# Kernel tuning notes

Hardware: AMD Instinct MI355X
Metric: run time of the kernel (lower is better)

## Reference

```python
import jax
import jax.numpy as jnp
import numpy as np

B, S, D, H, HID, E, TOPK = 1, 2048, 1024, 16, 4096, 8, 2
HEAD_DIM = D // H


def _layer_norm(x, g, b, eps=1e-5):
    mu = jnp.mean(x, axis=-1, keepdims=True)
    var = jnp.var(x, axis=-1, keepdims=True)
    return (x - mu) * jax.lax.rsqrt(var + eps) * g + b


def setup_inputs() -> dict:
    key = jax.random.key(0)
    ks = jax.random.split(key, 12)
    s = 0.02
    return {
        "x": jax.random.normal(ks[0], (B, S, D), jnp.float32),
        "ln1_g": jnp.ones((D,), jnp.float32),
        "ln1_b": jnp.zeros((D,), jnp.float32),
        "wq": jax.random.normal(ks[1], (D, D), jnp.float32) * s,
        "wk": jax.random.normal(ks[2], (D, D), jnp.float32) * s,
        "wv": jax.random.normal(ks[3], (D, D), jnp.float32) * s,
        "wo": jax.random.normal(ks[4], (D, D), jnp.float32) * s,
        "ln2_g": jnp.ones((D,), jnp.float32),
        "ln2_b": jnp.zeros((D,), jnp.float32),
        "w_gate": jax.random.normal(ks[5], (D, E), jnp.float32) * s,
        "w_eg": jax.random.normal(ks[6], (E, D, HID), jnp.float32) * s,
        "w_eu": jax.random.normal(ks[7], (E, D, HID), jnp.float32) * s,
        "w_ed": jax.random.normal(ks[8], (E, HID, D), jnp.float32) * s,
    }


def _attention(h, wq, wk, wv, wo):
    b, s, d = h.shape
    q = (h @ wq).reshape(b, s, H, HEAD_DIM).transpose(0, 2, 1, 3)
    k = (h @ wk).reshape(b, s, H, HEAD_DIM).transpose(0, 2, 1, 3)
    v = (h @ wv).reshape(b, s, H, HEAD_DIM).transpose(0, 2, 1, 3)
    scores = jnp.einsum("bhqd,bhkd->bhqk", q, k) / jnp.sqrt(jnp.asarray(HEAD_DIM, h.dtype))
    causal = jnp.tril(jnp.ones((s, s), bool))  # [s,s]
    scores = jnp.where(causal, scores, jnp.asarray(-1e30, h.dtype))
    attn = jax.nn.softmax(scores, axis=-1)
    out = jnp.einsum("bhqk,bhkd->bhqd", attn, v).transpose(0, 2, 1, 3).reshape(b, s, d)
    return out @ wo


def _moe(h, w_gate, w_eg, w_eu, w_ed):
    b, s, d = h.shape
    flat = h.reshape(-1, d)  # [T,D]
    logits = flat @ w_gate  # [T,E]
    scores = jax.nn.sigmoid(logits)
    top_val, top_idx = jax.lax.top_k(scores, TOPK)
    top_val = top_val / (jnp.sum(top_val, axis=-1, keepdims=True) + 1e-9)
    # per-token per-expert combine weight (0 for unrouted experts)
    combine = jnp.sum(jax.nn.one_hot(top_idx, E, dtype=flat.dtype) * top_val[..., None], axis=1)  # [T,E]
    g = jax.nn.silu(jnp.einsum("td,edh->eth", flat, w_eg))
    u = jnp.einsum("td,edh->eth", flat, w_eu)
    eo = jnp.einsum("eth,ehd->etd", g * u, w_ed)  # [E,T,D]
    out = jnp.einsum("etd,te->td", eo, combine)
    return out.reshape(b, s, d)


def reference(x, ln1_g, ln1_b, wq, wk, wv, wo, ln2_g, ln2_b, w_gate, w_eg, w_eu, w_ed):
    x = x + _attention(_layer_norm(x, ln1_g, ln1_b), wq, wk, wv, wo)
    x = x + _moe(_layer_norm(x, ln2_g, ln2_b), w_gate, w_eg, w_eu, w_ed)
    return x
```

## Files before the change

kernel.cpp:

```cpp
#include <hip/hip_runtime.h>
#include <hip/hip_bf16.h>
#include <stdint.h>

#define DI __device__ __forceinline__

typedef short bf16x8_t __attribute__((ext_vector_type(8)));
typedef float f32x4_t __attribute__((ext_vector_type(4)));

DI unsigned short f2bf(float f) {
  __hip_bfloat16 h = __float2bfloat16(f);
  unsigned short u;
  __builtin_memcpy(&u, &h, 2);
  return u;
}

DI uint32_t pk2(float a, float b) {
  return (uint32_t)f2bf(a) | ((uint32_t)f2bf(b) << 16);
}

DI f32x4_t mfma16(bf16x8_t a, bf16x8_t b, f32x4_t c) {
  return __builtin_amdgcn_mfma_f32_16x16x32_bf16(a, b, c, 0, 0, 0);
}

DI void gload16(const void* g, void* l) {
  __builtin_amdgcn_global_load_lds(
      (const __attribute__((address_space(1))) uint32_t*)g,
      (__attribute__((address_space(3))) uint32_t*)l, 16, 0, 0);
}

DI bf16x8_t frag(const unsigned short* base, int row, int hi) {
  return *(const bf16x8_t*)&base[row * 32 + ((hi ^ ((row >> 1) & 3)) * 8)];
}
DI int chunk_swz(int tid) { return ((tid & 3) ^ ((tid >> 3) & 3)) * 8; }

__global__ __launch_bounds__(256) void transpose_cvt(const float* __restrict__ in,
                                                     unsigned short* __restrict__ out,
                                                     int R, int C) {
  __shared__ float tile[64][65];
  const int tid = threadIdx.x;
  const int tx = tid & 15, ty = tid >> 4;
  const size_t zoff = (size_t)blockIdx.z * R * C;
  const int r0 = blockIdx.y * 64, c0 = blockIdx.x * 64;
#pragma unroll
  for (int i = 0; i < 4; ++i) {
    const int r = ty + i * 16;
    const float4 v = *(const float4*)(in + zoff + (size_t)(r0 + r) * C + c0 + tx * 4);
    tile[r][tx * 4 + 0] = v.x; tile[r][tx * 4 + 1] = v.y;
    tile[r][tx * 4 + 2] = v.z; tile[r][tx * 4 + 3] = v.w;
  }
  __syncthreads();
#pragma unroll
  for (int i = 0; i < 4; ++i) {
    const int r = ty + i * 16;
    ushort4 o;
    o.x = f2bf(tile[tx * 4 + 0][r]); o.y = f2bf(tile[tx * 4 + 1][r]);
    o.z = f2bf(tile[tx * 4 + 2][r]); o.w = f2bf(tile[tx * 4 + 3][r]);
    *(ushort4*)(out + zoff + (size_t)(c0 + r) * R + r0 + tx * 4) = o;
  }
}

__global__ __launch_bounds__(256) void ln_kernel(const float* __restrict__ x, const float* __restrict__ g,
                                                 const float* __restrict__ b, unsigned short* __restrict__ out) {
  const int row = blockIdx.x, tid = threadIdx.x;
  const int wid = tid >> 6, lane = tid & 63;
  const float4 v = *(const float4*)(x + (size_t)row * 1024 + tid * 4);
  float s = v.x + v.y + v.z + v.w;
  float s2 = v.x * v.x + v.y * v.y + v.z * v.z + v.w * v.w;
#pragma unroll
  for (int o = 1; o < 64; o <<= 1) { s += __shfl_xor(s, o); s2 += __shfl_xor(s2, o); }
  __shared__ float red[8];
  if (lane == 0) { red[wid] = s; red[4 + wid] = s2; }
  __syncthreads();
  const float ts = red[0] + red[1] + red[2] + red[3];
  const float ts2 = red[4] + red[5] + red[6] + red[7];
  const float mu = ts * 0.0009765625f;
  const float var = ts2 * 0.0009765625f - mu * mu;
  const float rs = rsqrtf(var + 1e-5f);
  const float4 gg = *(const float4*)(g + tid * 4);
  const float4 bb = *(const float4*)(b + tid * 4);
  ushort4 o4;
  o4.x = f2bf((v.x - mu) * rs * gg.x + bb.x);
  o4.y = f2bf((v.y - mu) * rs * gg.y + bb.y);
  o4.z = f2bf((v.z - mu) * rs * gg.z + bb.z);
  o4.w = f2bf((v.w - mu) * rs * gg.w + bb.w);
  *(ushort4*)(out + (size_t)row * 1024 + tid * 4) = o4;
}

template<int BN>
DI void gemm_loop(const unsigned short* aR0, const unsigned short* aR1,
                  const unsigned short* bR0, const unsigned short* bR1,
                  const int K, unsigned short* lds, const int tid,
                  f32x4_t (&acc)[4][BN / 32]) {
  constexpr int NF = BN / 32;
  unsigned short* ldsA = lds;
  unsigned short* ldsB = lds + 4096;
  const int wid = tid >> 6, lane = tid & 63, ln = lane & 15, hi = lane >> 4;
  const int wr = wid >> 1, wc = wid & 1;
  char* dstA0 = (char*)ldsA + wid * 1024;
  char* dstA1 = (char*)ldsA + 4096 + wid * 1024;
  char* dstB0 = (char*)ldsB + wid * 1024;
  char* dstB1 = (char*)ldsB + 4096 + wid * 1024;
  for (int k0 = 0; k0 < K; k0 += 32) {
    gload16(aR0 + k0, dstA0);
    gload16(aR1 + k0, dstA1);
    gload16(bR0 + k0, dstB0);
    if constexpr (BN == 128) gload16(bR1 + k0, dstB1);
    __syncthreads();
    bf16x8_t af[4];
#pragma unroll
    for (int mf = 0; mf < 4; ++mf)
      af[mf] = frag(ldsA, wr * 64 + mf * 16 + ln, hi);
#pragma unroll
    for (int nf = 0; nf < NF; ++nf) {
      bf16x8_t bfr = frag(ldsB, wc * (BN / 2) + nf * 16 + ln, hi);
#pragma unroll
      for (int mf = 0; mf < 4; ++mf)
        acc[mf][nf] = mfma16(af[mf], bfr, acc[mf][nf]);
    }
    __syncthreads();
  }
}

__global__ __launch_bounds__(256) void qkv_kernel(const unsigned short* __restrict__ h1,
                                                  const unsigned short* __restrict__ wqT,
                                                  const unsigned short* __restrict__ wkT,
                                                  const unsigned short* __restrict__ wvT,
                                                  unsigned short* __restrict__ qb,
                                                  unsigned short* __restrict__ kbf,
                                                  unsigned short* __restrict__ vt) {
  __shared__ unsigned short lds[128 * 32 + 128 * 32];
  const int tid = threadIdx.x;
  const int z = blockIdx.z;
  const unsigned short* BT = (z == 0) ? wqT : (z == 1) ? wkT : wvT;
  const int m0 = blockIdx.y * 128, n0 = blockIdx.x * 128;
  f32x4_t acc[4][4] = {};
  const int cs = chunk_swz(tid);
  const unsigned short* aR0 = h1 + (size_t)(m0 + (tid >> 2)) * 1024 + cs;
  const unsigned short* aR1 = aR0 + 64 * 1024;
  const unsigned short* bR0 = BT + (size_t)(n0 + (tid >> 2)) * 1024 + cs;
  const unsigned short* bR1 = bR0 + 64 * 1024;
  gemm_loop<128>(aR0, aR1, bR0, bR1, 1024, lds, tid, acc);
  const int lane = tid & 63, ln = lane & 15, hi = lane >> 4, wid = tid >> 6;
  const int wr = wid >> 1, wc = wid & 1;
  if (z < 2) {
    unsigned short* o = z ? kbf : qb;
#pragma unroll
    for (int mf = 0; mf < 4; ++mf)
#pragma unroll
      for (int nf = 0; nf < 4; ++nf)
#pragma unroll
        for (int r = 0; r < 4; ++r) {
          const int m = m0 + wr * 64 + mf * 16 + hi * 4 + r;
          const int n = n0 + wc * 64 + nf * 16 + ln;
          o[(size_t)m * 1024 + n] = f2bf(acc[mf][nf][r]);
        }
  } else {
#pragma unroll
    for (int mf = 0; mf < 4; ++mf)
#pragma unroll
      for (int nf = 0; nf < 4; ++nf) {
        const int n = n0 + wc * 64 + nf * 16 + ln;
        const int mb = m0 + wr * 64 + mf * 16 + hi * 4;
        ushort4 o;
        o.x = f2bf(acc[mf][nf][0]); o.y = f2bf(acc[mf][nf][1]);
        o.z = f2bf(acc[mf][nf][2]); o.w = f2bf(acc[mf][nf][3]);
        *(ushort4*)(vt + (size_t)n * 2048 + mb) = o;
      }
  }
}

__global__ __launch_bounds__(256) void wo_kernel(const unsigned short* __restrict__ ao,
                                                 const unsigned short* __restrict__ woT,
                                                 const float* __restrict__ x,
                                                 float* __restrict__ out) {
  __shared__ unsigned short lds[128 * 32 + 64 * 32];
  const int tid = threadIdx.x;
  const int m0 = blockIdx.y * 128, n0 = blockIdx.x * 64;
  f32x4_t acc[4][2] = {};
  const int cs = chunk_swz(tid);
  const unsigned short* aR0 = ao + (size_t)(m0 + (tid >> 2)) * 1024 + cs;
  const unsigned short* aR1 = aR0 + 64 * 1024;
  const unsigned short* bR0 = woT + (size_t)(n0 + (tid >> 2)) * 1024 + cs;
  gemm_loop<64>(aR0, aR1, bR0, nullptr, 1024, lds, tid, acc);
  const int lane = tid & 63, ln = lane & 15, hi = lane >> 4, wid = tid >> 6;
  const int wr = wid >> 1, wc = wid & 1;
#pragma unroll
  for (int mf = 0; mf < 4; ++mf)
#pragma unroll
    for (int nf = 0; nf < 2; ++nf)
#pragma unroll
      for (int r = 0; r < 4; ++r) {
        const int m = m0 + wr * 64 + mf * 16 + hi * 4 + r;
        const int n = n0 + wc * 32 + nf * 16 + ln;
        out[(size_t)m * 1024 + n] = acc[mf][nf][r] + x[(size_t)m * 1024 + n];
      }
}

__global__ __launch_bounds__(256) void attn_kernel(const unsigned short* __restrict__ qb,
                                                   const unsigned short* __restrict__ kbuf,
                                                   const unsigned short* __restrict__ vt,
                                                   unsigned short* __restrict__ ao) {
  __shared__ unsigned short kTl[4096];
  __shared__ unsigned short vTl[4096];
  __shared__ unsigned short pl[4][1024];
  const int tid = threadIdx.x;
  const int wid = tid >> 6, lane = tid & 63;
  const int ln = lane & 15, hi = lane >> 4;
  const int h = blockIdx.y;
  const int q0 = blockIdx.x * 64;
  const int q0w = q0 + wid * 16;

  const unsigned short* qrow = qb + (size_t)(q0w + ln) * 1024 + h * 64 + hi * 8;
  const bf16x8_t aq0 = *(const bf16x8_t*)(qrow);
  const bf16x8_t aq1 = *(const bf16x8_t*)(qrow + 32);

  const int str_r = tid >> 3, str_c = tid & 7;
  const int swc = (str_c ^ (str_r & 7)) * 8;
  const unsigned short* ksrc0 = kbuf + (size_t)str_r * 1024 + h * 64 + swc;
  const unsigned short* ksrc1 = kbuf + (size_t)(str_r + 32) * 1024 + h * 64 + swc;
  const unsigned short* vsrc0 = vt + (size_t)(h * 64 + str_r) * 2048 + swc;
  const unsigned short* vsrc1 = vt + (size_t)(h * 64 + str_r + 32) * 2048 + swc;
  char* kd0 = (char*)kTl + wid * 1024;
  char* kd1 = (char*)kTl + 4096 + wid * 1024;
  char* vd0 = (char*)vTl + wid * 1024;
  char* vd1 = (char*)vTl + 4096 + wid * 1024;

  float m_r[4], l_r[4];
  f32x4_t o_acc[4] = {};
#pragma unroll
  for (int r = 0; r < 4; ++r) { m_r[r] = -1e30f; l_r[r] = 0.f; }

  const int nkv = blockIdx.x + 1;
  for (int it = 0; it < nkv; ++it) {
    const int kv0 = it * 64;
    gload16(ksrc0 + (size_t)kv0 * 1024, kd0);
    gload16(ksrc1 + (size_t)kv0 * 1024, kd1);
    gload16(vsrc0 + kv0, vd0);
    gload16(vsrc1 + kv0, vd1);
    __syncthreads();

    float sc[4][4];
#pragma unroll
    for (int cf = 0; cf < 4; ++cf) {
      const int row = cf * 16 + ln;
      const int swz = row & 7;
      const bf16x8_t b0 = *(const bf16x8_t*)((char*)kTl + row * 128 + ((hi ^ swz) * 16));
      const bf16x8_t b1 = *(const bf16x8_t*)((char*)kTl + row * 128 + (((4 + hi) ^ swz) * 16));
      f32x4_t zacc = {};
      zacc = mfma16(aq0, b0, zacc);
      zacc = mfma16(aq1, b1, zacc);
#pragma unroll
      for (int r = 0; r < 4; ++r) sc[cf][r] = zacc[r] * 0.125f;
    }
    if (kv0 + 63 > q0w) {
#pragma unroll
      for (int cf = 0; cf < 4; ++cf)
#pragma unroll
        for (int r = 0; r < 4; ++r) {
          const int qg = q0w + hi * 4 + r;
          const int kg = kv0 + cf * 16 + ln;
          if (kg > qg) sc[cf][r] = -1e30f;
        }
    }
#pragma unroll
    for (int r = 0; r < 4; ++r) {
      float tm = fmaxf(fmaxf(sc[0][r], sc[1][r]), fmaxf(sc[2][r], sc[3][r]));
      tm = fmaxf(tm, __shfl_xor(tm, 1));
      tm = fmaxf(tm, __shfl_xor(tm, 2));
      tm = fmaxf(tm, __shfl_xor(tm, 4));
      tm = fmaxf(tm, __shfl_xor(tm, 8));
      const float mn = fmaxf(m_r[r], tm);
      const float alpha = __expf(m_r[r] - mn);
      float rsum = 0.f;
#pragma unroll
      for (int cf = 0; cf < 4; ++cf) {
        const float p = __expf(sc[cf][r] - mn);
        sc[cf][r] = p; rsum += p;
      }
      rsum += __shfl_xor(rsum, 1); rsum += __shfl_xor(rsum, 2);
      rsum += __shfl_xor(rsum, 4); rsum += __shfl_xor(rsum, 8);
      l_r[r] = l_r[r] * alpha + rsum;
      m_r[r] = mn;
#pragma unroll
      for (int df = 0; df < 4; ++df) o_acc[df][r] *= alpha;
    }
    unsigned short* pw = &pl[wid][0];
#pragma unroll
    for (int cf = 0; cf < 4; ++cf)
#pragma unroll
      for (int r = 0; r < 4; ++r) {
        const int qq = hi * 4 + r;
        const int kv = cf * 16 + ln;
        const int bo = (qq * 128 + kv * 2) ^ ((qq & 7) << 4);
        *(unsigned short*)((char*)pw + bo) = f2bf(sc[cf][r]);
      }
    __syncthreads();
    const bf16x8_t pa0 = *(const bf16x8_t*)((char*)pw + ((ln * 128 + hi * 16) ^ ((ln & 7) << 4)));
    const bf16x8_t pa1 = *(const bf16x8_t*)((char*)pw + ((ln * 128 + 64 + hi * 16) ^ ((ln & 7) << 4)));
#pragma unroll
    for (int df = 0; df < 4; ++df) {
      const int d = df * 16 + ln;
      const int swz = d & 7;
      const bf16x8_t bv0 = *(const bf16x8_t*)((char*)vTl + d * 128 + ((hi ^ swz) * 16));
      const bf16x8_t bv1 = *(const bf16x8_t*)((char*)vTl + d * 128 + (((4 + hi) ^ swz) * 16));
      o_acc[df] = mfma16(pa0, bv0, o_acc[df]);
      o_acc[df] = mfma16(pa1, bv1, o_acc[df]);
    }
    __syncthreads();
  }
#pragma unroll
  for (int df = 0; df < 4; ++df) {
    const int n = h * 64 + df * 16 + ln;
#pragma unroll
    for (int r = 0; r < 4; ++r) {
      const int m = q0w + hi * 4 + r;
      ao[(size_t)m * 1024 + n] = f2bf(o_acc[df][r] / l_r[r]);
    }
  }
}

__global__ __launch_bounds__(256) void gate_kernel(const float* __restrict__ x2, const float* __restrict__ g,
                                                   const float* __restrict__ b, const float* __restrict__ wg,
                                                   int2* __restrict__ te, float2* __restrict__ tw,
                                                   int* __restrict__ cnt) {
  const int tid = threadIdx.x, wid = tid >> 6, lane = tid & 63;
  const int t = blockIdx.x * 4 + wid;
  const float* row = x2 + (size_t)t * 1024;
  float vv[16];
#pragma unroll
  for (int i = 0; i < 4; ++i) *(float4*)&vv[i * 4] = *(const float4*)(row + lane * 16 + i * 4);
  float s = 0.f, s2 = 0.f;
#pragma unroll
  for (int j = 0; j < 16; ++j) { s += vv[j]; s2 += vv[j] * vv[j]; }
#pragma unroll
  for (int o = 1; o < 64; o <<= 1) { s += __shfl_xor(s, o); s2 += __shfl_xor(s2, o); }
  const float mu = s * 0.0009765625f;
  const float var = s2 * 0.0009765625f - mu * mu;
  const float rs = rsqrtf(var + 1e-5f);
  float acc[8] = {0.f, 0.f, 0.f, 0.f, 0.f, 0.f, 0.f, 0.f};
#pragma unroll
  for (int j = 0; j < 16; ++j) {
    const int d = lane * 16 + j;
    const float xv = (vv[j] - mu) * rs * g[d] + b[d];
    const float4 w0 = *(const float4*)(wg + d * 8);
    const float4 w1 = *(const float4*)(wg + d * 8 + 4);
    acc[0] += xv * w0.x; acc[1] += xv * w0.y; acc[2] += xv * w0.z; acc[3] += xv * w0.w;
    acc[4] += xv * w1.x; acc[5] += xv * w1.y; acc[6] += xv * w1.z; acc[7] += xv * w1.w;
  }
#pragma unroll
  for (int o = 1; o < 64; o <<= 1) {
#pragma unroll
    for (int e = 0; e < 8; ++e) acc[e] += __shfl_xor(acc[e], o);
  }
  if (lane == 0) {
    float sg[8];
#pragma unroll
    for (int e = 0; e < 8; ++e) sg[e] = 1.f / (1.f + __expf(-acc[e]));
    int e0 = 0;
#pragma unroll
    for (int e = 1; e < 8; ++e) if (sg[e] > sg[e0]) e0 = e;
    int e1 = (e0 == 0) ? 1 : 0;
#pragma unroll
    for (int e = 0; e < 8; ++e) if (e != e0 && sg[e] > sg[e1]) e1 = e;
    const float v0 = sg[e0], v1 = sg[e1];
    const float inv = 1.f / (v0 + v1 + 1e-9f);
    te[t] = make_int2(e0, e1);
    tw[t] = make_float2(v0 * inv, v1 * inv);
    atomicAdd(&cnt[e0], 1);
    atomicAdd(&cnt[e1], 1);
  }
}

__global__ void zero_counters(int* p) { if (threadIdx.x < 8) p[threadIdx.x] = 0; }

__global__ void g2_kernel(const int* __restrict__ cnt, int* __restrict__ slot_off,
                          int* __restrict__ tile_expert, int* __restrict__ tile_rowbase,
                          int* __restrict__ cursor, int* __restrict__ assign_token,
                          float* __restrict__ assign_w) {
  const int tid = threadIdx.x;
  for (int i = tid; i < 5120; i += 64) { assign_token[i] = -1; assign_w[i] = 0.f; }
  if (tid == 0) {
    int base = 0, tiles = 0;
    for (int e = 0; e < 8; ++e) {
      const int c = cnt[e];
      slot_off[e] = base;
      cursor[e] = 0;
      const int nt = (c + 127) >> 7;
      for (int i = 0; i < nt; ++i) {
        tile_expert[tiles] = e;
        tile_rowbase[tiles] = base + i * 128;
        ++tiles;
      }
      base += nt * 128;
    }
    for (; tiles < 40; ++tiles) tile_expert[tiles] = -1;
  }
}

__global__ __launch_bounds__(256) void g3_kernel(const int2* __restrict__ te, const float2* __restrict__ tw,
                                                 const int* __restrict__ slot_off, int* __restrict__ cursor,
                                                 int* __restrict__ assign_token, float* __restrict__ assign_w) {
  const int t = blockIdx.x * 256 + threadIdx.x;
  const int2 e = te[t];
  const float2 w = tw[t];
  const int s0 = slot_off[e.x] + atomicAdd(&cursor[e.x], 1);
  assign_token[s0] = t; assign_w[s0] = w.x;
  const int s1 = slot_off[e.y] + atomicAdd(&cursor[e.y], 1);
  assign_token[s1] = t; assign_w[s1] = w.y;
}

__global__ __launch_bounds__(256) void upgate_kernel(const unsigned short* __restrict__ h2,
                                                     const float* __restrict__ w_eg, const float* __restrict__ w_eu,
                                                     const int* __restrict__ tile_expert,
                                                     const int* __restrict__ tile_rowbase,
                                                     const int* __restrict__ assign_token,
                                                     unsigned short* __restrict__ act) {
  const int by = blockIdx.y;
  const int e = tile_expert[by];
  if (e < 0) return;
  const int n0 = blockIdx.x * 64;
  const int rowbase = tile_rowbase[by];
  const int tid = threadIdx.x;
  __shared__ unsigned short lds[2 * 4096 + 2 * 4096];
  unsigned short* ldsA = lds;
  unsigned short* ldsB = lds + 8192;
  const int wid = tid >> 6, lane = tid & 63, ln = lane & 15, hi = lane >> 4;
  const int wr = wid >> 1, wc = wid & 1;
  const int r0s = rowbase + (tid >> 2);
  int t0 = assign_token[r0s];       t0 = t0 < 0 ? 0 : t0;
  int t1 = assign_token[r0s + 64];  t1 = t1 < 0 ? 0 : t1;
  const int cs = chunk_swz(tid);
  const unsigned short* aR0 = h2 + (size_t)t0 * 1024 + cs;
  const unsigned short* aR1 = h2 + (size_t)t1 * 1024 + cs;
  const int mat = tid >> 7;
  const int blk = tid & 127;
  const int kb = (blk >> 4) * 4;
  const int nb = (blk & 15) * 4;
  const float* bsrc = (mat ? w_eu : w_eg) + (size_t)e * 1024 * 4096 + (size_t)kb * 4096 + n0 + nb;
  int boff[4];
#pragma unroll
  for (int i = 0; i < 4; ++i) {
    const int n = nb + i;
    int bo = mat * 4096 + n * 64 + kb * 2;
    bo ^= ((n >> 2) & 7) << 4;
    boff[i] = bo;
  }
  f32x4_t accg[4][2] = {};
  f32x4_t accu[4][2] = {};
  gload16(aR0, (char*)ldsA + wid * 1024);
  gload16(aR1, (char*)ldsA + 4096 + wid * 1024);
  {
    const float4 q0 = *(const float4*)(bsrc);
    const float4 q1 = *(const float4*)(bsrc + 4096);
    const float4 q2 = *(const float4*)(bsrc + 8192);
    const float4 q3 = *(const float4*)(bsrc + 12288);
    const float* q0p = (const float*)&q0; const float* q1p = (const float*)&q1;
    const float* q2p = (const float*)&q2; const float* q3p = (const float*)&q3;
#pragma unroll
    for (int i = 0; i < 4; ++i) {
      uint2 w;
      w.x = pk2(q0p[i], q1p[i]);
      w.y = pk2(q2p[i], q3p[i]);
      *(uint2*)((char*)ldsB + boff[i]) = w;
    }
  }
  __syncthreads();
  int buf = 0;
  for (int k0 = 0; k0 < 1024; k0 += 32) {
    const int kn = k0 + 32;
    const int nbuf = buf ^ 1;
    const bool pf = kn < 1024;
    float4 q0, q1, q2, q3;
    if (pf) {
      gload16(aR0 + kn, (char*)ldsA + nbuf * 8192 + wid * 1024);
      gload16(aR1 + kn, (char*)ldsA + nbuf * 8192 + 4096 + wid * 1024);
      const float* bs = bsrc + (size_t)kn * 4096;
      q0 = *(const float4*)(bs);
      q1 = *(const float4*)(bs + 4096);
      q2 = *(const float4*)(bs + 8192);
      q3 = *(const float4*)(bs + 12288);
    }
    const unsigned short* A = ldsA + buf * 4096;
    const char* Bb = (char*)ldsB + buf * 8192;
    bf16x8_t af[4];
#pragma unroll
    for (int mf = 0; mf < 4; ++mf)
      af[mf] = frag(A, wr * 64 + mf * 16 + ln, hi);
#pragma unroll
    for (int nf = 0; nf < 2; ++nf) {
      const int nrow = wc * 32 + nf * 16 + ln;
      int bo = nrow * 64 + hi * 16;
      bo ^= ((nrow >> 2) & 7) << 4;
      const bf16x8_t bg = *(const bf16x8_t*)(Bb + bo);
      const bf16x8_t bu = *(const bf16x8_t*)(Bb + 4096 + bo);
#pragma unroll
      for (int mf = 0; mf < 4; ++mf) {
        accg[mf][nf] = mfma16(af[mf], bg, accg[mf][nf]);
        accu[mf][nf] = mfma16(af[mf], bu, accu[mf][nf]);
      }
    }
    if (pf) {
      char* Bn = (char*)ldsB + nbuf * 8192;
      const float* q0p = (const float*)&q0; const float* q1p = (const float*)&q1;
      const float* q2p = (const float*)&q2; const float* q3p = (const float*)&q3;
#pragma unroll
      for (int i = 0; i < 4; ++i) {
        uint2 w;
        w.x = pk2(q0p[i], q1p[i]);
        w.y = pk2(q2p[i], q3p[i]);
        *(uint2*)(Bn + boff[i]) = w;
      }
    }
    __syncthreads();
    buf = nbuf;
  }
#pragma unroll
  for (int mf = 0; mf < 4; ++mf)
#pragma unroll
    for (int nf = 0; nf < 2; ++nf)
#pragma unroll
      for (int r = 0; r < 4; ++r) {
        const int m = wr * 64 + mf * 16 + hi * 4 + r;
        const int n = n0 + wc * 32 + nf * 16 + ln;
        const float gv = accg[mf][nf][r], uv = accu[mf][nf][r];
        const float val = gv / (1.f + __expf(-gv)) * uv;
        act[(size_t)(rowbase + m) * 4096 + n] = f2bf(val);
      }
}

__global__ __launch_bounds__(256) void down_kernel(const unsigned short* __restrict__ act,
                                                   const float* __restrict__ w_ed,
                                                   const int* __restrict__ tile_expert,
                                                   const int* __restrict__ tile_rowbase,
                                                   const int* __restrict__ assign_token,
                                                   const float* __restrict__ assign_w,
                                                   float* __restrict__ out) {
  const int by = blockIdx.y;
  const int e = tile_expert[by];
  if (e < 0) return;
  const int n0 = blockIdx.x * 64;
  const int rowbase = tile_rowbase[by];
  const int tid = threadIdx.x;
  __shared__ unsigned short lds[2 * 4096 + 2 * 2048];
  unsigned short* ldsA = lds;
  unsigned short* ldsB = lds + 8192;
  const int wid = tid >> 6, lane = tid & 63, ln = lane & 15, hi = lane >> 4;
  const int wr = wid >> 1, wc = wid & 1;
  const int cs = chunk_swz(tid);
  const unsigned short* aR0 = act + (size_t)(rowbase + (tid >> 2)) * 4096 + cs;
  const unsigned short* aR1 = aR0 + (size_t)64 * 4096;
  const int nb = (tid & 15) * 4;
  const int kb2 = (tid >> 4) * 2;
  const float* bsrc = w_ed + (size_t)e * 4096 * 1024 + (size_t)kb2 * 1024 + n0 + nb;
  int boff[4];
#pragma unroll
  for (int i = 0; i < 4; ++i) {
    const int n = nb + i;
    int bo = n * 64 + kb2 * 2;
    bo ^= ((n >> 2) & 7) << 4;
    boff[i] = bo;
  }
  f32x4_t acc[4][2] = {};
  gload16(aR0, (char*)ldsA + wid * 1024);
  gload16(aR1, (char*)ldsA + 4096 + wid * 1024);
  {
    const float4 q0 = *(const float4*)(bsrc);
    const float4 q1 = *(const float4*)(bsrc + 1024);
    const float* q0p = (const float*)&q0; const float* q1p = (const float*)&q1;
#pragma unroll
    for (int i = 0; i < 4; ++i)
      *(uint32_t*)((char*)ldsB + boff[i]) = pk2(q0p[i], q1p[i]);
  }
  __syncthreads();
  int buf = 0;
  for (int k0 = 0; k0 < 4096; k0 += 32) {
    const int kn = k0 + 32;
    const int nbuf = buf ^ 1;
    const bool pf = kn < 4096;
    float4 q0, q1;
    if (pf) {
      gload16(aR0 + kn, (char*)ldsA + nbuf * 8192 + wid * 1024);
      gload16(aR1 + kn, (char*)ldsA + nbuf * 8192 + 4096 + wid * 1024);
      const float* bs = bsrc + (size_t)kn * 1024;
      q0 = *(const float4*)(bs);
      q1 = *(const float4*)(bs + 1024);
    }
    const unsigned short* A = ldsA + buf * 4096;
    const char* Bb = (char*)ldsB + buf * 4096;
    bf16x8_t af[4];
#pragma unroll
    for (int mf = 0; mf < 4; ++mf)
      af[mf] = frag(A, wr * 64 + mf * 16 + ln, hi);
#pragma unroll
    for (int nf = 0; nf < 2; ++nf) {
      const int nrow = wc * 32 + nf * 16 + ln;
      int bo = nrow * 64 + hi * 16;
      bo ^= ((nrow >> 2) & 7) << 4;
      const bf16x8_t bb = *(const bf16x8_t*)(Bb + bo);
#pragma unroll
      for (int mf = 0; mf < 4; ++mf)
        acc[mf][nf] = mfma16(af[mf], bb, acc[mf][nf]);
    }
    if (pf) {
      char* Bn = (char*)ldsB + nbuf * 4096;
      const float* q0p = (const float*)&q0; const float* q1p = (const float*)&q1;
#pragma unroll
      for (int i = 0; i < 4; ++i)
        *(uint32_t*)(Bn + boff[i]) = pk2(q0p[i], q1p[i]);
    }
    __syncthreads();
    buf = nbuf;
  }
#pragma unroll
  for (int mf = 0; mf < 4; ++mf)
#pragma unroll
    for (int r = 0; r < 4; ++r) {
      const int m = wr * 64 + mf * 16 + hi * 4 + r;
      const int slot = rowbase + m;
      const int tk = assign_token[slot];
      if (tk >= 0) {
        const float w = assign_w[slot];
#pragma unroll
        for (int nf = 0; nf < 2; ++nf) {
          const int n = n0 + wc * 32 + nf * 16 + ln;
          atomicAdd(out + (size_t)tk * 1024 + n, acc[mf][nf][r] * w);
        }
      }
    }
}

extern "C" void kernel_launch(void* const* d_in, const int* in_sizes, int n_in,
                              void* d_out, int out_size, void* d_ws, size_t ws_size,
                              hipStream_t stream) {
  (void)in_sizes; (void)n_in; (void)out_size;
  const float* x    = (const float*)d_in[0];
  const float* ln1g = (const float*)d_in[1];
  const float* ln1b = (const float*)d_in[2];
  const float* wq   = (const float*)d_in[3];
  const float* wk   = (const float*)d_in[4];
  const float* wv   = (const float*)d_in[5];
  const float* wo   = (const float*)d_in[6];
  const float* ln2g = (const float*)d_in[7];
  const float* ln2b = (const float*)d_in[8];
  const float* wg   = (const float*)d_in[9];
  const float* weg  = (const float*)d_in[10];
  const float* weu  = (const float*)d_in[11];
  const float* wed  = (const float*)d_in[12];
  float* out = (float*)d_out;
  char* ws = (char*)d_ws;

  const size_t MB = (size_t)1 << 20;
  if (ws_size < 74 * MB) return;
  unsigned short* wqT = (unsigned short*)(ws + 0 * MB);
  unsigned short* wkT = (unsigned short*)(ws + 2 * MB);
  unsigned short* wvT = (unsigned short*)(ws + 4 * MB);
  unsigned short* woT = (unsigned short*)(ws + 6 * MB);
  unsigned short* h1  = (unsigned short*)(ws + 8 * MB);
  unsigned short* qb  = (unsigned short*)(ws + 12 * MB);
  unsigned short* kbf = (unsigned short*)(ws + 16 * MB);
  unsigned short* vt  = (unsigned short*)(ws + 20 * MB);
  unsigned short* ao  = (unsigned short*)(ws + 24 * MB);
  unsigned short* h2  = (unsigned short*)(ws + 28 * MB);
  unsigned short* act = (unsigned short*)(ws + 32 * MB);
  int2*   te = (int2*)(ws + 72 * MB);
  float2* tw = (float2*)(ws + 72 * MB + 16384);
  int*  meta = (int*)(ws + 72 * MB + 32768);
  int* cnt = meta;
  int* cursor = meta + 8;
  int* slot_off = meta + 16;
  int* tile_expert = meta + 24;
  int* tile_rowbase = meta + 64;
  int*   assign_token = (int*)(ws + 72 * MB + 36864);
  float* assign_w     = (float*)(ws + 72 * MB + 36864 + 20480);

  zero_counters<<<1, 64, 0, stream>>>(cnt);
  transpose_cvt<<<dim3(16, 16, 1), 256, 0, stream>>>(wq, wqT, 1024, 1024);
  transpose_cvt<<<dim3(16, 16, 1), 256, 0, stream>>>(wk, wkT, 1024, 1024);
  transpose_cvt<<<dim3(16, 16, 1), 256, 0, stream>>>(wv, wvT, 1024, 1024);
  transpose_cvt<<<dim3(16, 16, 1), 256, 0, stream>>>(wo, woT, 1024, 1024);
  ln_kernel<<<2048, 256, 0, stream>>>(x, ln1g, ln1b, h1);
  qkv_kernel<<<dim3(8, 16, 3), 256, 0, stream>>>(h1, wqT, wkT, wvT, qb, kbf, vt);
  attn_kernel<<<dim3(32, 16), 256, 0, stream>>>(qb, kbf, vt, ao);
  wo_kernel<<<dim3(16, 16), 256, 0, stream>>>(ao, woT, x, out);
  ln_kernel<<<2048, 256, 0, stream>>>(out, ln2g, ln2b, h2);
  gate_kernel<<<512, 256, 0, stream>>>(out, ln2g, ln2b, wg, te, tw, cnt);
  g2_kernel<<<1, 64, 0, stream>>>(cnt, slot_off, tile_expert, tile_rowbase, cursor, assign_token, assign_w);
  g3_kernel<<<8, 256, 0, stream>>>(te, tw, slot_off, cursor, assign_token, assign_w);
  upgate_kernel<<<dim3(64, 40), 256, 0, stream>>>(h2, weg, weu, tile_expert, tile_rowbase, assign_token, act);
  down_kernel<<<dim3(16, 40), 256, 0, stream>>>(act, wed, tile_expert, tile_rowbase, assign_token, assign_w, out);
}
```

Baseline: 525.6 us.

## Deepen MoE GEMM pipelines to four A stages with explicit waitcnt scheduling

Result: slower. 536.3 us (+2.0%).

```diff
diff --git a/kernel.cpp b/kernel.cpp
--- a/kernel.cpp
+++ b/kernel.cpp
@@ -409,6 +409,67 @@
   assign_token[s1] = t; assign_w[s1] = w.y;
 }
 
+struct Q4u { float4 a, b, c, d; };
+struct Q2d { float4 a, b; };
+
+DI void ug_write_b(char* Bn, const int* boff, const Q4u& q) {
+  const float* q0p = (const float*)&q.a; const float* q1p = (const float*)&q.b;
+  const float* q2p = (const float*)&q.c; const float* q3p = (const float*)&q.d;
+#pragma unroll
+  for (int i = 0; i < 4; ++i) {
+    uint2 w;
+    w.x = pk2(q0p[i], q1p[i]);
+    w.y = pk2(q2p[i], q3p[i]);
+    *(uint2*)(Bn + boff[i]) = w;
+  }
+}
+
+DI void ug_mfma(const unsigned short* A, const char* Bb, int wr, int wc, int ln, int hi,
+                f32x4_t (&accg)[4][2], f32x4_t (&accu)[4][2]) {
+  bf16x8_t af[4];
+#pragma unroll
+  for (int mf = 0; mf < 4; ++mf)
+    af[mf] = frag(A, wr * 64 + mf * 16 + ln, hi);
+#pragma unroll
+  for (int nf = 0; nf < 2; ++nf) {
+    const int nrow = wc * 32 + nf * 16 + ln;
+    int bo = nrow * 64 + hi * 16;
+    bo ^= ((nrow >> 2) & 7) << 4;
+    const bf16x8_t bg = *(const bf16x8_t*)(Bb + bo);
+    const bf16x8_t bu = *(const bf16x8_t*)(Bb + 4096 + bo);
+#pragma unroll
+    for (int mf = 0; mf < 4; ++mf) {
+      accg[mf][nf] = mfma16(af[mf], bg, accg[mf][nf]);
+      accu[mf][nf] = mfma16(af[mf], bu, accu[mf][nf]);
+    }
+  }
+}
+
+template<bool PF>
+DI void ug_step(const float* bs2, const unsigned short* a0n, const unsigned short* a1n,
+                char* A_pf, Q4u& qld, const Q4u& qwr, char* B_nxt, const int* boff,
+                const unsigned short* A_cur, const char* B_cur,
+                int wr, int wc, int ln, int hi, int wid,
+                f32x4_t (&accg)[4][2], f32x4_t (&accu)[4][2]) {
+  if constexpr (PF) {
+    qld.a = *(const float4*)(bs2);
+    qld.b = *(const float4*)(bs2 + 4096);
+    qld.c = *(const float4*)(bs2 + 8192);
+    qld.d = *(const float4*)(bs2 + 12288);
+    gload16(a0n, A_pf + wid * 1024);
+    gload16(a1n, A_pf + 4096 + wid * 1024);
+    __builtin_amdgcn_sched_barrier(0);
+  }
+  ug_write_b(B_nxt, boff, qwr);
+  ug_mfma(A_cur, B_cur, wr, wc, ln, hi, accg, accu);
+  if constexpr (PF) asm volatile("s_waitcnt vmcnt(6)" ::: "memory");
+  else              asm volatile("s_waitcnt vmcnt(0)" ::: "memory");
+  __builtin_amdgcn_sched_barrier(0);
+  asm volatile("s_waitcnt lgkmcnt(0)" ::: "memory");
+  __builtin_amdgcn_sched_barrier(0);
+  __builtin_amdgcn_s_barrier();
+}
+
 __global__ __launch_bounds__(256) void upgate_kernel(const unsigned short* __restrict__ h2,
                                                      const float* __restrict__ w_eg, const float* __restrict__ w_eu,
                                                      const int* __restrict__ tile_expert,
@@ -421,9 +482,7 @@
   const int n0 = blockIdx.x * 64;
   const int rowbase = tile_rowbase[by];
   const int tid = threadIdx.x;
-  __shared__ unsigned short lds[2 * 4096 + 2 * 4096];
-  unsigned short* ldsA = lds;
-  unsigned short* ldsB = lds + 8192;
+  __shared__ unsigned short lds[4 * 4096 + 2 * 4096];
   const int wid = tid >> 6, lane = tid & 63, ln = lane & 15, hi = lane >> 4;
   const int wr = wid >> 1, wc = wid & 1;
   const int r0s = rowbase + (tid >> 2);
@@ -445,75 +504,58 @@
     bo ^= ((n >> 2) & 7) << 4;
     boff[i] = bo;
   }
+  char* Ab[4] = {(char*)lds, (char*)lds + 8192, (char*)lds + 16384, (char*)lds + 24576};
+  char* B0 = (char*)lds + 32768;
+  char* B1 = (char*)lds + 40960;
   f32x4_t accg[4][2] = {};
   f32x4_t accu[4][2] = {};
-  gload16(aR0, (char*)ldsA + wid * 1024);
-  gload16(aR1, (char*)ldsA + 4096 + wid * 1024);
+  Q4u q0, q1;
+  q0.a = *(const float4*)(bsrc);
+  q0.b = *(const float4*)(bsrc + 4096);
+  q0.c = *(const float4*)(bsrc + 8192);
+  q0.d = *(const float4*)(bsrc + 12288);
+  gload16(aR0, Ab[0] + wid * 1024);
+  gload16(aR1, Ab[0] + 4096 + wid * 1024);
+  __builtin_amdgcn_sched_barrier(0);
+  ug_write_b(B0, boff, q0);
   {
-    const float4 q0 = *(const float4*)(bsrc);
-    const float4 q1 = *(const float4*)(bsrc + 4096);
-    const float4 q2 = *(const float4*)(bsrc + 8192);
-    const float4 q3 = *(const float4*)(bsrc + 12288);
-    const float* q0p = (const float*)&q0; const float* q1p = (const float*)&q1;
-    const float* q2p = (const float*)&q2; const float* q3p = (const float*)&q3;
-#pragma unroll
-    for (int i = 0; i < 4; ++i) {
-      uint2 w;
-      w.x = pk2(q0p[i], q1p[i]);
-      w.y = pk2(q2p[i], q3p[i]);
-      *(uint2*)((char*)ldsB + boff[i]) = w;
-    }
-  }
-  __syncthreads();
-  int buf = 0;
-  for (int k0 = 0; k0 < 1024; k0 += 32) {
-    const int kn = k0 + 32;
-    const int nbuf = buf ^ 1;
-    const bool pf = kn < 1024;
-    float4 q0, q1, q2, q3;
-    if (pf) {
-      gload16(aR0 + kn, (char*)ldsA + nbuf * 8192 + wid * 1024);
-      gload16(aR1 + kn, (char*)ldsA + nbuf * 8192 + 4096 + wid * 1024);
-      const float* bs = bsrc + (size_t)kn * 4096;
-      q0 = *(const float4*)(bs);
-      q1 = *(const float4*)(bs + 4096);
-      q2 = *(const float4*)(bs + 8192);
-      q3 = *(const float4*)(bs + 12288);
-    }
-    const unsigned short* A = ldsA + buf * 4096;
-    const char* Bb = (char*)ldsB + buf * 8192;
-    bf16x8_t af[4];
-#pragma unroll
-    for (int mf = 0; mf < 4; ++mf)
-      af[mf] = frag(A, wr * 64 + mf * 16 + ln, hi);
-#pragma unroll
-    for (int nf = 0; nf < 2; ++nf) {
-      const int nrow = wc * 32 + nf * 16 + ln;
-      int bo = nrow * 64 + hi * 16;
-      bo ^= ((nrow >> 2) & 7) << 4;
-      const bf16x8_t bg = *(const bf16x8_t*)(Bb + bo);
-      const bf16x8_t bu = *(const bf16x8_t*)(Bb + 4096 + bo);
-#pragma unroll
-      for (int mf = 0; mf < 4; ++mf) {
-        accg[mf][nf] = mfma16(af[mf], bg, accg[mf][nf]);
-        accu[mf][nf] = mfma16(af[mf], bu, accu[mf][nf]);
-      }
-    }
-    if (pf) {
-      char* Bn = (char*)ldsB + nbuf * 8192;
-      const float* q0p = (const float*)&q0; const float* q1p = (const float*)&q1;
-      const float* q2p = (const float*)&q2; const float* q3p = (const float*)&q3;
-#pragma unroll
-      for (int i = 0; i < 4; ++i) {
-        uint2 w;
-        w.x = pk2(q0p[i], q1p[i]);
-        w.y = pk2(q2p[i], q3p[i]);
-        *(uint2*)(Bn + boff[i]) = w;
-      }
-    }
-    __syncthreads();
-    buf = nbuf;
-  }
+    const float* bs = bsrc + (size_t)32 * 4096;
+    q1.a = *(const float4*)(bs);
+    q1.b = *(const float4*)(bs + 4096);
+    q1.c = *(const float4*)(bs + 8192);
+    q1.d = *(const float4*)(bs + 12288);
+  }
+  gload16(aR0 + 32, Ab[1] + wid * 1024);
+  gload16(aR1 + 32, Ab[1] + 4096 + wid * 1024);
+  asm volatile("s_waitcnt vmcnt(6)" ::: "memory");
+  __builtin_amdgcn_sched_barrier(0);
+  asm volatile("s_waitcnt lgkmcnt(0)" ::: "memory");
+  __builtin_amdgcn_sched_barrier(0);
+  __builtin_amdgcn_s_barrier();
+  for (int p = 0; p < 7; ++p) {
+    const int t = p * 4;
+    ug_step<true>(bsrc + (size_t)(t + 2) * 32 * 4096, aR0 + (t + 2) * 32, aR1 + (t + 2) * 32,
+                  Ab[2], q0, q1, B1, boff, (const unsigned short*)Ab[0], B0,
+                  wr, wc, ln, hi, wid, accg, accu);
+    ug_step<true>(bsrc + (size_t)(t + 3) * 32 * 4096, aR0 + (t + 3) * 32, aR1 + (t + 3) * 32,
+                  Ab[3], q1, q0, B0, boff, (const unsigned short*)Ab[1], B1,
+                  wr, wc, ln, hi, wid, accg, accu);
+    ug_step<true>(bsrc + (size_t)(t + 4) * 32 * 4096, aR0 + (t + 4) * 32, aR1 + (t + 4) * 32,
+                  Ab[0], q0, q1, B1, boff, (const unsigned short*)Ab[2], B0,
+                  wr, wc, ln, hi, wid, accg, accu);
+    ug_step<true>(bsrc + (size_t)(t + 5) * 32 * 4096, aR0 + (t + 5) * 32, aR1 + (t + 5) * 32,
+                  Ab[1], q1, q0, B0, boff, (const unsigned short*)Ab[3], B1,
+                  wr, wc, ln, hi, wid, accg, accu);
+  }
+  ug_step<true>(bsrc + (size_t)30 * 32 * 4096, aR0 + 30 * 32, aR1 + 30 * 32,
+                Ab[2], q0, q1, B1, boff, (const unsigned short*)Ab[0], B0,
+                wr, wc, ln, hi, wid, accg, accu);
+  ug_step<true>(bsrc + (size_t)31 * 32 * 4096, aR0 + 31 * 32, aR1 + 31 * 32,
+                Ab[3], q1, q0, B0, boff, (const unsigned short*)Ab[1], B1,
+                wr, wc, ln, hi, wid, accg, accu);
+  ug_step<false>(nullptr, nullptr, nullptr, nullptr, q0, q1, B1, boff,
+                 (const unsigned short*)Ab[2], B0, wr, wc, ln, hi, wid, accg, accu);
+  ug_mfma((const unsigned short*)Ab[3], B1, wr, wc, ln, hi, accg, accu);
 #pragma unroll
   for (int mf = 0; mf < 4; ++mf)
 #pragma unroll
@@ -526,6 +568,54 @@
         const float val = gv / (1.f + __expf(-gv)) * uv;
         act[(size_t)(rowbase + m) * 4096 + n] = f2bf(val);
       }
+}
+
+DI void dn_write_b(char* Bn, const int* boff, const Q2d& q) {
+  const float* q0p = (const float*)&q.a; const float* q1p = (const float*)&q.b;
+#pragma unroll
+  for (int i = 0; i < 4; ++i)
+    *(uint32_t*)(Bn + boff[i]) = pk2(q0p[i], q1p[i]);
+}
+
+DI void dn_mfma(const unsigned short* A, const char* Bb, int wr, int wc, int ln, int hi,
+                f32x4_t (&acc)[4][2]) {
+  bf16x8_t af[4];
+#pragma unroll
+  for (int mf = 0; mf < 4; ++mf)
+    af[mf] = frag(A, wr * 64 + mf * 16 + ln, hi);
+#pragma unroll
+  for (int nf = 0; nf < 2; ++nf) {
+    const int nrow = wc * 32 + nf * 16 + ln;
+    int bo = nrow * 64 + hi * 16;
+    bo ^= ((nrow >> 2) & 7) << 4;
+    const bf16x8_t bb = *(const bf16x8_t*)(Bb + bo);
+#pragma unroll
+    for (int mf = 0; mf < 4; ++mf)
+      acc[mf][nf] = mfma16(af[mf], bb, acc[mf][nf]);
+  }
+}
+
+template<bool PF>
+DI void dn_step(const float* bs2, const unsigned short* a0n, const unsigned short* a1n,
+                char* A_pf, Q2d& qld, const Q2d& qwr, char* B_nxt, const int* boff,
+                const unsigned short* A_cur, const char* B_cur,
+                int wr, int wc, int ln, int hi, int wid,
+                f32x4_t (&acc)[4][2]) {
+  if constexpr (PF) {
+    qld.a = *(const float4*)(bs2);
+    qld.b = *(const float4*)(bs2 + 1024);
+    gload16(a0n, A_pf + wid * 1024);
+    gload16(a1n, A_pf + 4096 + wid * 1024);
+    __builtin_amdgcn_sched_barrier(0);
+  }
+  dn_write_b(B_nxt, boff, qwr);
+  dn_mfma(A_cur, B_cur, wr, wc, ln, hi, acc);
+  if constexpr (PF) asm volatile("s_waitcnt vmcnt(4)" ::: "memory");
+  else              asm volatile("s_waitcnt vmcnt(0)" ::: "memory");
+  __builtin_amdgcn_sched_barrier(0);
+  asm volatile("s_waitcnt lgkmcnt(0)" ::: "memory");
+  __builtin_amdgcn_sched_barrier(0);
+  __builtin_amdgcn_s_barrier();
 }
 
 __global__ __launch_bounds__(256) void down_kernel(const unsigned short* __restrict__ act,
@@ -541,9 +631,7 @@
   const int n0 = blockIdx.x * 64;
   const int rowbase = tile_rowbase[by];
   const int tid = threadIdx.x;
-  __shared__ unsigned short lds[2 * 4096 + 2 * 2048];
-  unsigned short* ldsA = lds;
-  unsigned short* ldsB = lds + 8192;
+  __shared__ unsigned short lds[4 * 4096 + 2 * 2048];
   const int wid = tid >> 6, lane = tid & 63, ln = lane & 15, hi = lane >> 4;
   const int wr = wid >> 1, wc = wid & 1;
   const int cs = chunk_swz(tid);
@@ -560,57 +648,53 @@
     bo ^= ((n >> 2) & 7) << 4;
     boff[i] = bo;
   }
+  char* Ab[4] = {(char*)lds, (char*)lds + 8192, (char*)lds + 16384, (char*)lds + 24576};
+  char* B0 = (char*)lds + 32768;
+  char* B1 = (char*)lds + 36864;
   f32x4_t acc[4][2] = {};
-  gload16(aR0, (char*)ldsA + wid * 1024);
-  gload16(aR1, (char*)ldsA + 4096 + wid * 1024);
+  Q2d q0, q1;
+  q0.a = *(const float4*)(bsrc);
+  q0.b = *(const float4*)(bsrc + 1024);
+  gload16(aR0, Ab[0] + wid * 1024);
+  gload16(aR1, Ab[0] + 4096 + wid * 1024);
+  __builtin_amdgcn_sched_barrier(0);
+  dn_write_b(B0, boff, q0);
   {
-    const float4 q0 = *(const float4*)(bsrc);
-    const float4 q1 = *(const float4*)(bsrc + 1024);
-    const float* q0p = (const float*)&q0; const float* q1p = (const float*)&q1;
-#pragma unroll
-    for (int i = 0; i < 4; ++i)
-      *(uint32_t*)((char*)ldsB + boff[i]) = pk2(q0p[i], q1p[i]);
-  }
-  __syncthreads();
-  int buf = 0;
-  for (int k0 = 0; k0 < 4096; k0 += 32) {
-    const int kn = k0 + 32;
-    const int nbuf = buf ^ 1;
-    const bool pf = kn < 4096;
-    float4 q0, q1;
-    if (pf) {
-      gload16(aR0 + kn, (char*)ldsA + nbuf * 8192 + wid * 1024);
-      gload16(aR1 + kn, (char*)ldsA + nbuf * 8192 + 4096 + wid * 1024);
-      const float* bs = bsrc + (size_t)kn * 1024;
-      q0 = *(const float4*)(bs);
-      q1 = *(const float4*)(bs + 1024);
-    }
-    const unsigned short* A = ldsA + buf * 4096;
-    const char* Bb = (char*)ldsB + buf * 4096;
-    bf16x8_t af[4];
-#pragma unroll
-    for (int mf = 0; mf < 4; ++mf)
-      af[mf] = frag(A, wr * 64 + mf * 16 + ln, hi);
-#pragma unroll
-    for (int nf = 0; nf < 2; ++nf) {
-      const int nrow = wc * 32 + nf * 16 + ln;
-      int bo = nrow * 64 + hi * 16;
-      bo ^= ((nrow >> 2) & 7) << 4;
-      const bf16x8_t bb = *(const bf16x8_t*)(Bb + bo);
-#pragma unroll
-      for (int mf = 0; mf < 4; ++mf)
-        acc[mf][nf] = mfma16(af[mf], bb, acc[mf][nf]);
-    }
-    if (pf) {
-      char* Bn = (char*)ldsB + nbuf * 4096;
-      const float* q0p = (const float*)&q0; const float* q1p = (const float*)&q1;
-#pragma unroll
-      for (int i = 0; i < 4; ++i)
-        *(uint32_t*)(Bn + boff[i]) = pk2(q0p[i], q1p[i]);
-    }
-    __syncthreads();
-    buf = nbuf;
-  }
+    const float* bs = bsrc + (size_t)32 * 1024;
+    q1.a = *(const float4*)(bs);
+    q1.b = *(const float4*)(bs + 1024);
+  }
+  gload16(aR0 + 32, Ab[1] + wid * 1024);
+  gload16(aR1 + 32, Ab[1] + 4096 + wid * 1024);
+  asm volatile("s_waitcnt vmcnt(4)" ::: "memory");
+  __builtin_amdgcn_sched_barrier(0);
+  asm volatile("s_waitcnt lgkmcnt(0)" ::: "memory");
+  __builtin_amdgcn_sched_barrier(0);
+  __builtin_amdgcn_s_barrier();
+  for (int p = 0; p < 31; ++p) {
+    const int t = p * 4;
+    dn_step<true>(bsrc + (size_t)(t + 2) * 32 * 1024, aR0 + (t + 2) * 32, aR1 + (t + 2) * 32,
+                  Ab[2], q0, q1, B1, boff, (const unsigned short*)Ab[0], B0,
+                  wr, wc, ln, hi, wid, acc);
+    dn_step<true>(bsrc + (size_t)(t + 3) * 32 * 1024, aR0 + (t + 3) * 32, aR1 + (t + 3) * 32,
+                  Ab[3], q1, q0, B0, boff, (const unsigned short*)Ab[1], B1,
+                  wr, wc, ln, hi, wid, acc);
+    dn_step<true>(bsrc + (size_t)(t + 4) * 32 * 1024, aR0 + (t + 4) * 32, aR1 + (t + 4) * 32,
+                  Ab[0], q0, q1, B1, boff, (const unsigned short*)Ab[2], B0,
+                  wr, wc, ln, hi, wid, acc);
+    dn_step<true>(bsrc + (size_t)(t + 5) * 32 * 1024, aR0 + (t + 5) * 32, aR1 + (t + 5) * 32,
+                  Ab[1], q1, q0, B0, boff, (const unsigned short*)Ab[3], B1,
+                  wr, wc, ln, hi, wid, acc);
+  }
+  dn_step<true>(bsrc + (size_t)126 * 32 * 1024, aR0 + 126 * 32, aR1 + 126 * 32,
+                Ab[2], q0, q1, B1, boff, (const unsigned short*)Ab[0], B0,
+                wr, wc, ln, hi, wid, acc);
+  dn_step<true>(bsrc + (size_t)127 * 32 * 1024, aR0 + 127 * 32, aR1 + 127 * 32,
+                Ab[3], q1, q0, B0, boff, (const unsigned short*)Ab[1], B1,
+                wr, wc, ln, hi, wid, acc);
+  dn_step<false>(nullptr, nullptr, nullptr, nullptr, q0, q1, B1, boff,
+                 (const unsigned short*)Ab[2], B0, wr, wc, ln, hi, wid, acc);
+  dn_mfma((const unsigned short*)Ab[3], B1, wr, wc, ln, hi, acc);
 #pragma unroll
   for (int mf = 0; mf < 4; ++mf)
 #pragma unroll
```
